# Optimization experiments

Hardware: AMD Instinct MI355X
Metric: run time of the kernel (lower is better)

Reference implementation:

```python
import jax, jax.numpy as jnp
import numpy as np
import math

W = 256      # attention_window
DIL = 1      # attention_dilation
H = 12       # num heads
HD = 64      # head dim
E = 768      # hidden size


def setup_inputs() -> dict:
    key = jax.random.key(0)
    ks = jax.random.split(key, 4)
    B, S = 2, 4096
    s = 0.02
    inp = {"hidden_states": jax.random.normal(ks[0], (B, S, E), jnp.float32)}
    inp["Wq"] = jax.random.normal(ks[1], (E, E), jnp.float32) * s
    inp["Wk"] = jax.random.normal(ks[2], (E, E), jnp.float32) * s
    inp["Wv"] = jax.random.normal(ks[3], (E, E), jnp.float32) * s
    inp["bq"] = jnp.zeros((E,), jnp.float32)
    inp["bk"] = jnp.zeros((E,), jnp.float32)
    inp["bv"] = jnp.zeros((E,), jnp.float32)
    return inp


def _banded_attention(q, k, v):
    # q,k,v: [B,S,H,HD]; banded attention with window W, dilation DIL
    B, S, Hh, D = q.shape
    offsets = (jnp.arange(2 * W + 1) - W) * DIL  # relative key offsets
    pos = jnp.arange(S)

    def score(off):
        idx = pos + off
        valid = (idx >= 0) & (idx < S)          # mask_invalid_locations
        kk = k[:, jnp.clip(idx, 0, S - 1)]      # [B,S,H,HD] shifted keys
        s = jnp.einsum('bshd,bshd->bsh', q, kk)
        return jnp.where(valid[None, :, None], s, -jnp.inf)

    # diagonaled_mm(q, k): [2W+1, B, S, H] -> [B, S, H, 2W+1]
    scores = jax.lax.map(score, offsets)
    probs = jax.nn.softmax(jnp.moveaxis(scores, 0, -1), axis=-1)

    # diagonaled_mm(probs, v, is_t1_diagonaled=True): accumulate over band
    def step(acc, j):
        off = offsets[j]
        idx = pos + off
        valid = (idx >= 0) & (idx < S)
        vv = v[:, jnp.clip(idx, 0, S - 1)]
        p = jnp.where(valid[None, :, None], probs[..., j], 0.0)
        return acc + p[..., None] * vv, None

    out, _ = jax.lax.scan(step, jnp.zeros_like(v), jnp.arange(2 * W + 1))
    return out


def reference(hidden_states, Wq, bq, Wk, bk, Wv, bv):
    B, S, _ = hidden_states.shape
    q = (hidden_states @ Wq.T + bq) / math.sqrt(HD)
    k = hidden_states @ Wk.T + bk
    v = hidden_states @ Wv.T + bv
    q = q.reshape(B, S, H, HD)
    k = k.reshape(B, S, H, HD)
    v = v.reshape(B, S, H, HD)
    out = _banded_attention(q, k, v)  # [B,S,H,HD]
    return out.reshape(B, S, E)
```

## Files before the change

kernel.cpp:

```cpp
#include <hip/hip_runtime.h>

#define S_LEN 4096
#define BATCH 2
#define EMB   768
#define NH    12
#define HDIM  64
#define WIN   256

using f32x4  = __attribute__((ext_vector_type(4))) float;
using bf16x8 = __attribute__((ext_vector_type(8))) short;
using u16x8  = __attribute__((ext_vector_type(8))) unsigned short;

#define AS1 __attribute__((address_space(1)))
#define AS3 __attribute__((address_space(3)))

__device__ __forceinline__ unsigned short f2bf(float x) {
    unsigned int u = __float_as_uint(x);
    return (unsigned short)((u + 0x7fffu + ((u >> 16) & 1u)) >> 16);
}

__global__ void cvt_kernel(const float* __restrict__ in,
                           unsigned short* __restrict__ out, int n8) {
    int i = blockIdx.x * blockDim.x + threadIdx.x;
    if (i >= n8) return;
    const float4* p = reinterpret_cast<const float4*>(in) + (size_t)i * 2;
    float4 a = p[0];
    float4 b = p[1];
    u16x8 o;
    o[0] = f2bf(a.x); o[1] = f2bf(a.y); o[2] = f2bf(a.z); o[3] = f2bf(a.w);
    o[4] = f2bf(b.x); o[5] = f2bf(b.y); o[6] = f2bf(b.z); o[7] = f2bf(b.w);
    reinterpret_cast<u16x8*>(out)[i] = o;
}

__global__ void cvt3_kernel(const float* __restrict__ w0, const float* __restrict__ w1,
                            const float* __restrict__ w2,
                            unsigned short* __restrict__ o0, unsigned short* __restrict__ o1,
                            unsigned short* __restrict__ o2, int n8) {
    int i = blockIdx.x * blockDim.x + threadIdx.x;
    if (i >= n8) return;
    const float* in = (blockIdx.y == 0) ? w0 : (blockIdx.y == 1) ? w1 : w2;
    unsigned short* out = (blockIdx.y == 0) ? o0 : (blockIdx.y == 1) ? o1 : o2;
    const float4* p = reinterpret_cast<const float4*>(in) + (size_t)i * 2;
    float4 a = p[0];
    float4 b = p[1];
    u16x8 o;
    o[0] = f2bf(a.x); o[1] = f2bf(a.y); o[2] = f2bf(a.z); o[3] = f2bf(a.w);
    o[4] = f2bf(b.x); o[5] = f2bf(b.y); o[6] = f2bf(b.z); o[7] = f2bf(b.w);
    reinterpret_cast<u16x8*>(out)[i] = o;
}

#define NKT (EMB / 32)

__global__ __launch_bounds__(256) void qkv_gemm(
    const unsigned short* __restrict__ A,
    const unsigned short* __restrict__ Wq,
    const unsigned short* __restrict__ Wk,
    const unsigned short* __restrict__ Wv,
    const float* __restrict__ bq,
    const float* __restrict__ bk,
    const float* __restrict__ bv,
    unsigned short* __restrict__ qo,
    unsigned short* __restrict__ ko,
    unsigned short* __restrict__ vo)
{
    __shared__ unsigned short As[4][128 * 32];
    __shared__ unsigned short Bs[4][128 * 32];

    const int tid  = threadIdx.x;
    const int lane = tid & 63;
    const int wave = tid >> 6;
    const int mblk = blockIdx.x;
    const int nblk = blockIdx.y;
    const int wsel = nblk / 6;
    const int nloc0 = (nblk % 6) * 128;
    const unsigned short* Wp = (wsel == 0) ? Wq : ((wsel == 1) ? Wk : Wv);
    const int wm = wave >> 1, wn = wave & 1;

    f32x4 acc[4][4];
#pragma unroll
    for (int i = 0; i < 4; ++i)
#pragma unroll
        for (int j = 0; j < 4; ++j)
            acc[i][j] = (f32x4){0.f, 0.f, 0.f, 0.f};

    const int frow = lane & 15;
    const int g    = lane >> 4;

    const char* Abase = (const char*)(A  + (size_t)(mblk * 128) * EMB);
    const char* Bbase = (const char*)(Wp + (size_t)nloc0 * EMB);

    const int srow = tid >> 2;
    const int pb   = tid & 3;
    const int sblk = pb ^ (srow & 3);

#define GLDS(gp, lp) __builtin_amdgcn_global_load_lds((const AS1 unsigned int*)(gp), (AS3 unsigned int*)(lp), 16, 0, 0)
#define STG_A(q, t) do {                                                                                 \
    GLDS(Abase + (size_t)srow * 1536 + (t) * 64 + sblk * 16,        &As[q][srow * 32 + pb * 8]);         \
    GLDS(Abase + (size_t)(64 + srow) * 1536 + (t) * 64 + sblk * 16, &As[q][(64 + srow) * 32 + pb * 8]);  \
} while (0)
#define STG_B(q, t) do {                                                                                 \
    GLDS(Bbase + (size_t)srow * 1536 + (t) * 64 + sblk * 16,        &Bs[q][srow * 32 + pb * 8]);         \
    GLDS(Bbase + (size_t)(64 + srow) * 1536 + (t) * 64 + sblk * 16, &Bs[q][(64 + srow) * 32 + pb * 8]);  \
} while (0)

    auto rdA = [&](int q, int mi) -> bf16x8 {
        int r = wm * 64 + mi * 16 + frow;
        return *reinterpret_cast<const bf16x8*>(&As[q][r * 32 + (g ^ (r & 3)) * 8]);
    };
    auto rdB = [&](int q, int ni) -> bf16x8 {
        int r = wn * 64 + ni * 16 + frow;
        return *reinterpret_cast<const bf16x8*>(&Bs[q][r * 32 + (g ^ (r & 3)) * 8]);
    };

    STG_A(0, 0); STG_B(0, 0);
    STG_A(1, 1); STG_B(1, 1);
    STG_A(2, 2); STG_B(2, 2);
    asm volatile("s_waitcnt vmcnt(8)" ::: "memory");
    asm volatile("s_barrier" ::: "memory");

#define WINDOW(t, DO_STAGE) do {                                                              \
    const int q_ = (t) & 3;                                                                   \
    bf16x8 afr[4], bfr[4];                                                                    \
    _Pragma("unroll") for (int ni = 0; ni < 4; ++ni) bfr[ni] = rdB(q_, ni);                   \
    _Pragma("unroll") for (int mi = 0; mi < 4; ++mi) afr[mi] = rdA(q_, mi);                   \
    if (DO_STAGE) { STG_A(((t) + 3) & 3, (t) + 3); STG_B(((t) + 3) & 3, (t) + 3); }           \
    __builtin_amdgcn_s_setprio(1);                                                            \
    _Pragma("unroll") for (int mi = 0; mi < 4; ++mi)                                          \
        _Pragma("unroll") for (int ni = 0; ni < 4; ++ni)                                      \
            acc[mi][ni] = __builtin_amdgcn_mfma_f32_16x16x32_bf16(afr[mi], bfr[ni], acc[mi][ni], 0, 0, 0); \
    __builtin_amdgcn_s_setprio(0);                                                            \
} while (0)

#pragma unroll 1
    for (int t = 0; t < NKT - 3; ++t) {
        WINDOW(t, true);
        asm volatile("s_waitcnt vmcnt(8)" ::: "memory");
        asm volatile("s_barrier" ::: "memory");
    }
    WINDOW(NKT - 3, false);
    asm volatile("s_waitcnt vmcnt(4)" ::: "memory");
    asm volatile("s_barrier" ::: "memory");
    WINDOW(NKT - 2, false);
    asm volatile("s_waitcnt vmcnt(0)" ::: "memory");
    asm volatile("s_barrier" ::: "memory");
    WINDOW(NKT - 1, false);

    const float* bias = (wsel == 0) ? bq : ((wsel == 1) ? bk : bv);
    const int rowg = g * 4;
#pragma unroll
    for (int mi = 0; mi < 4; ++mi) {
        int mbase = mblk * 128 + wm * 64 + mi * 16 + rowg;
#pragma unroll
        for (int ni = 0; ni < 4; ++ni) {
            int nl = nloc0 + wn * 64 + ni * 16 + frow;
            float bb = bias[nl];
            int h = nl >> 6, hd = nl & 63;
#pragma unroll
            for (int r = 0; r < 4; ++r) {
                int mm = mbase + r;
                int b = mm >> 12, s = mm & 4095;
                float v = acc[mi][ni][r] + bb;
                if (wsel == 0) {
                    v *= 0.125f;
                    qo[((size_t)(b * NH + h) * S_LEN + s) * HDIM + hd] = f2bf(v);
                } else if (wsel == 1) {
                    ko[((size_t)(b * NH + h) * S_LEN + s) * HDIM + hd] = f2bf(v);
                } else {
                    vo[((size_t)(b * NH + h) * HDIM + hd) * S_LEN + s] = f2bf(v);
                }
            }
        }
    }
}

#define QB   128
#define KC   64
#define NCHQ ((QB + 2 * WIN) / KC)

#define STAGE_ATT(buf, ks) do {                                                              \
    const unsigned short* kr_ = kp + (size_t)((ks) + srow) * HDIM + gblk * 8;                \
    __builtin_amdgcn_global_load_lds(                                                        \
        (const AS1 unsigned int*)kr_,                                                        \
        (AS3 unsigned int*)&Ksm[buf][wave * 512], 16, 0, 0);                                 \
    const unsigned short* vr_ = vp + (size_t)srow * S_LEN + (ks) + gblk * 8;                 \
    __builtin_amdgcn_global_load_lds(                                                        \
        (const AS1 unsigned int*)vr_,                                                        \
        (AS3 unsigned int*)&Vsm[buf][wave * 512], 16, 0, 0);                                 \
} while (0)

__global__ __launch_bounds__(512) void banded_attn(
    const unsigned short* __restrict__ qg,
    const unsigned short* __restrict__ kg,
    const unsigned short* __restrict__ vtg,
    float* __restrict__ out)
{
    __shared__ unsigned short Ksm[2][KC * HDIM];
    __shared__ unsigned short Vsm[2][HDIM * KC];
    __shared__ unsigned short Psm[8][16 * KC];

    const int tid  = threadIdx.x;
    const int wave = tid >> 6, lane = tid & 63;
    const int qb = blockIdx.x * QB;
    const int h  = blockIdx.y, b = blockIdx.z;

    const unsigned short* qp = qg  + (size_t)(b * NH + h) * S_LEN * HDIM;
    const unsigned short* kp = kg  + (size_t)(b * NH + h) * S_LEN * HDIM;
    const unsigned short* vp = vtg + (size_t)(b * NH + h) * HDIM * S_LEN;

    const int frow = lane & 15;
    const int g    = lane >> 4;
    const int fcol = g * 8;

    const int srow = tid >> 3;
    const int gblk = (tid & 7) ^ (srow & 7);

    bf16x8 qf[2];
    {
        const unsigned short* qr = qp + (size_t)(qb + wave * 16 + frow) * HDIM;
        qf[0] = *reinterpret_cast<const bf16x8*>(qr + fcol);
        qf[1] = *reinterpret_cast<const bf16x8*>(qr + 32 + fcol);
    }

    float l_part[4];
    f32x4 o_acc[4];
#pragma unroll
    for (int r = 0; r < 4; ++r) l_part[r] = 0.f;
#pragma unroll
    for (int ni = 0; ni < 4; ++ni) o_acc[ni] = (f32x4){0.f, 0.f, 0.f, 0.f};

    const int c_start = (qb < WIN) ? ((WIN - qb) >> 6) : 0;
    const int c_end   = min(NCHQ, (S_LEN + WIN - qb) >> 6);
    const int qrow0 = qb + wave * 16 + g * 4;

    const int w_lo = qb + wave * 16 - WIN;
    const int w_hi = qb + wave * 16 + 15 + WIN;

    STAGE_ATT(0, qb - WIN + c_start * KC);
    asm volatile("s_waitcnt vmcnt(0)" ::: "memory");
    __syncthreads();

    int cur = 0;
    for (int c = c_start; c < c_end; ++c) {
        const int ks = qb - WIN + c * KC;
        if (c + 1 < c_end) STAGE_ATT(cur ^ 1, ks + KC);

        const bool active = (ks + KC - 1 >= w_lo) && (ks <= w_hi);
        if (active) {
            f32x4 sc[4];
#pragma unroll
            for (int ni = 0; ni < 4; ++ni) sc[ni] = (f32x4){0.f, 0.f, 0.f, 0.f};
#pragma unroll
            for (int ni = 0; ni < 4; ++ni) {
                int krow = ni * 16 + frow;
                int sw   = (krow & 7) << 3;
                bf16x8 kf0 = *reinterpret_cast<const bf16x8*>(&Ksm[cur][krow * KC + (fcol ^ sw)]);
                bf16x8 kf1 = *reinterpret_cast<const bf16x8*>(&Ksm[cur][krow * KC + ((32 + fcol) ^ sw)]);
                sc[ni] = __builtin_amdgcn_mfma_f32_16x16x32_bf16(qf[0], kf0, sc[ni], 0, 0, 0);
                sc[ni] = __builtin_amdgcn_mfma_f32_16x16x32_bf16(qf[1], kf1, sc[ni], 0, 0, 0);
            }

            float pm[4][4];
#pragma unroll
            for (int ni = 0; ni < 4; ++ni) {
                int d0 = qrow0 - (ks + ni * 16 + frow);
#pragma unroll
                for (int r = 0; r < 4; ++r) {
                    bool valid = (unsigned)(d0 + r + WIN) <= (unsigned)(2 * WIN);
                    pm[ni][r] = valid ? __expf(sc[ni][r]) : 0.f;
                }
            }
#pragma unroll
            for (int r = 0; r < 4; ++r) {
                l_part[r] += (pm[0][r] + pm[1][r]) + (pm[2][r] + pm[3][r]);
                int prow = g * 4 + r;
#pragma unroll
                for (int ni = 0; ni < 4; ++ni) {
                    int pelem = (ni * 16 + frow) ^ ((prow & 7) << 3);
                    Psm[wave][prow * KC + pelem] = f2bf(pm[ni][r]);
                }
            }

            asm volatile("s_waitcnt lgkmcnt(0)" ::: "memory");
            __builtin_amdgcn_sched_barrier(0);

            bf16x8 pf[2];
#pragma unroll
            for (int kk = 0; kk < 2; ++kk) {
                int sw = (frow & 7) << 3;
                pf[kk] = *reinterpret_cast<const bf16x8*>(&Psm[wave][frow * KC + ((kk * 32 + fcol) ^ sw)]);
            }
#pragma unroll
            for (int ni = 0; ni < 4; ++ni) {
                int vrow = ni * 16 + frow;
                int sw   = (vrow & 7) << 3;
#pragma unroll
                for (int kk = 0; kk < 2; ++kk) {
                    bf16x8 vf = *reinterpret_cast<const bf16x8*>(&Vsm[cur][vrow * KC + ((kk * 32 + fcol) ^ sw)]);
                    o_acc[ni] = __builtin_amdgcn_mfma_f32_16x16x32_bf16(pf[kk], vf, o_acc[ni], 0, 0, 0);
                }
            }
        }

        asm volatile("s_waitcnt vmcnt(0)" ::: "memory");
        __syncthreads();
        cur ^= 1;
    }

#pragma unroll
    for (int d = 1; d < 16; d <<= 1)
#pragma unroll
        for (int r = 0; r < 4; ++r)
            l_part[r] += __shfl_xor(l_part[r], d, 64);

#pragma unroll
    for (int r = 0; r < 4; ++r) {
        float inv = 1.0f / l_part[r];
        int s = qrow0 + r;
        size_t obase = ((size_t)b * S_LEN + s) * EMB + h * HDIM;
#pragma unroll
        for (int ni = 0; ni < 4; ++ni)
            out[obase + ni * 16 + frow] = o_acc[ni][r] * inv;
    }
}

extern "C" void kernel_launch(void* const* d_in, const int* in_sizes, int n_in,
                              void* d_out, int out_size, void* d_ws, size_t ws_size,
                              hipStream_t stream) {
    const float* hs = (const float*)d_in[0];
    const float* Wq = (const float*)d_in[1];
    const float* Wk = (const float*)d_in[2];
    const float* Wv = (const float*)d_in[3];
    const float* bq = (const float*)d_in[4];
    const float* bk = (const float*)d_in[5];
    const float* bv = (const float*)d_in[6];
    float* out = (float*)d_out;

    char* w = (char*)d_ws;
    unsigned short* hs_bf = (unsigned short*)w;
    unsigned short* wq_bf = (unsigned short*)(w + 12582912);
    unsigned short* wk_bf = wq_bf + 589824;
    unsigned short* wv_bf = wk_bf + 589824;
    unsigned short* q_ws  = (unsigned short*)(w + 12582912 + 3 * 1179648);
    unsigned short* k_ws  = q_ws + 6291456;
    unsigned short* v_ws  = k_ws + 6291456;

    cvt_kernel<<<3072, 256, 0, stream>>>(hs, hs_bf, 786432);
    cvt3_kernel<<<dim3(288, 3), 256, 0, stream>>>(Wq, Wk, Wv, wq_bf, wk_bf, wv_bf, 73728);

    qkv_gemm<<<dim3(64, 18), 256, 0, stream>>>(hs_bf, wq_bf, wk_bf, wv_bf,
                                               bq, bk, bv, q_ws, k_ws, v_ws);

    banded_attn<<<dim3(S_LEN / QB, NH, BATCH), 512, 0, stream>>>(q_ws, k_ws, v_ws, out);
}
```

Before: 109.4 us.

## Rework QKV GEMM: swizzled block order, double buffering, vectorized transposed epilogue stores

The QKV projection GEMM remaps workgroup IDs so consecutive blocks share operand tiles in cache. It also changes the LDS swizzle pattern and replaces the 4-deep global_load_lds pipeline with a simpler double buffer that waits on vmcnt(0) each step. For Q and K it swaps the MFMA operand order, and for V it keeps the original order, so each lane holds 4 contiguous output elements. The epilogue can then write packed 4x bf16 stores instead of scalar 16-bit stores. The shallower pipeline and full waits each iteration may expose more load latency, while the halved LDS footprint may allow more resident blocks.

```diff
diff --git a/kernel.cpp b/kernel.cpp
--- a/kernel.cpp
+++ b/kernel.cpp
@@ -9,6 +9,7 @@
 
 using f32x4  = __attribute__((ext_vector_type(4))) float;
 using bf16x8 = __attribute__((ext_vector_type(8))) short;
+using u16x4  = __attribute__((ext_vector_type(4))) unsigned short;
 using u16x8  = __attribute__((ext_vector_type(8))) unsigned short;
 
 #define AS1 __attribute__((address_space(1)))
@@ -63,14 +64,17 @@
     unsigned short* __restrict__ ko,
     unsigned short* __restrict__ vo)
 {
-    __shared__ unsigned short As[4][128 * 32];
-    __shared__ unsigned short Bs[4][128 * 32];
+    __shared__ unsigned short As[2][128 * 32];
+    __shared__ unsigned short Bs[2][128 * 32];
 
     const int tid  = threadIdx.x;
     const int lane = tid & 63;
     const int wave = tid >> 6;
-    const int mblk = blockIdx.x;
-    const int nblk = blockIdx.y;
+
+    const int wg  = blockIdx.y * 64 + blockIdx.x;
+    const int v   = (wg & 7) * 144 + (wg >> 3);
+    const int mblk = v & 63;
+    const int nblk = v >> 6;
     const int wsel = nblk / 6;
     const int nloc0 = (nblk % 6) * 128;
     const unsigned short* Wp = (wsel == 0) ? Wq : ((wsel == 1) ? Wk : Wv);
@@ -91,83 +95,90 @@
 
     const int srow = tid >> 2;
     const int pb   = tid & 3;
-    const int sblk = pb ^ (srow & 3);
+    const int sblk = pb ^ ((srow >> 1) & 3);
 
 #define GLDS(gp, lp) __builtin_amdgcn_global_load_lds((const AS1 unsigned int*)(gp), (AS3 unsigned int*)(lp), 16, 0, 0)
-#define STG_A(q, t) do {                                                                                 \
+#define STG(q, t) do {                                                                                   \
     GLDS(Abase + (size_t)srow * 1536 + (t) * 64 + sblk * 16,        &As[q][srow * 32 + pb * 8]);         \
     GLDS(Abase + (size_t)(64 + srow) * 1536 + (t) * 64 + sblk * 16, &As[q][(64 + srow) * 32 + pb * 8]);  \
-} while (0)
-#define STG_B(q, t) do {                                                                                 \
     GLDS(Bbase + (size_t)srow * 1536 + (t) * 64 + sblk * 16,        &Bs[q][srow * 32 + pb * 8]);         \
     GLDS(Bbase + (size_t)(64 + srow) * 1536 + (t) * 64 + sblk * 16, &Bs[q][(64 + srow) * 32 + pb * 8]);  \
 } while (0)
 
     auto rdA = [&](int q, int mi) -> bf16x8 {
         int r = wm * 64 + mi * 16 + frow;
-        return *reinterpret_cast<const bf16x8*>(&As[q][r * 32 + (g ^ (r & 3)) * 8]);
+        return *reinterpret_cast<const bf16x8*>(&As[q][r * 32 + (g ^ ((r >> 1) & 3)) * 8]);
     };
     auto rdB = [&](int q, int ni) -> bf16x8 {
         int r = wn * 64 + ni * 16 + frow;
-        return *reinterpret_cast<const bf16x8*>(&Bs[q][r * 32 + (g ^ (r & 3)) * 8]);
+        return *reinterpret_cast<const bf16x8*>(&Bs[q][r * 32 + (g ^ ((r >> 1) & 3)) * 8]);
     };
 
-    STG_A(0, 0); STG_B(0, 0);
-    STG_A(1, 1); STG_B(1, 1);
-    STG_A(2, 2); STG_B(2, 2);
-    asm volatile("s_waitcnt vmcnt(8)" ::: "memory");
-    asm volatile("s_barrier" ::: "memory");
-
-#define WINDOW(t, DO_STAGE) do {                                                              \
-    const int q_ = (t) & 3;                                                                   \
-    bf16x8 afr[4], bfr[4];                                                                    \
-    _Pragma("unroll") for (int ni = 0; ni < 4; ++ni) bfr[ni] = rdB(q_, ni);                   \
-    _Pragma("unroll") for (int mi = 0; mi < 4; ++mi) afr[mi] = rdA(q_, mi);                   \
-    if (DO_STAGE) { STG_A(((t) + 3) & 3, (t) + 3); STG_B(((t) + 3) & 3, (t) + 3); }           \
-    __builtin_amdgcn_s_setprio(1);                                                            \
-    _Pragma("unroll") for (int mi = 0; mi < 4; ++mi)                                          \
-        _Pragma("unroll") for (int ni = 0; ni < 4; ++ni)                                      \
-            acc[mi][ni] = __builtin_amdgcn_mfma_f32_16x16x32_bf16(afr[mi], bfr[ni], acc[mi][ni], 0, 0, 0); \
-    __builtin_amdgcn_s_setprio(0);                                                            \
+#define KLOOP(SW) do {                                                                        \
+    STG(0, 0);                                                                                \
+    asm volatile("s_waitcnt vmcnt(0)" ::: "memory");                                          \
+    __syncthreads();                                                                          \
+    int cur = 0;                                                                              \
+    _Pragma("unroll 1")                                                                       \
+    for (int t = 0; t < NKT; ++t) {                                                           \
+        if (t + 1 < NKT) STG(cur ^ 1, t + 1);                                                 \
+        bf16x8 afr[4], bfr[4];                                                                \
+        _Pragma("unroll") for (int ni = 0; ni < 4; ++ni) bfr[ni] = rdB(cur, ni);              \
+        _Pragma("unroll") for (int mi = 0; mi < 4; ++mi) afr[mi] = rdA(cur, mi);              \
+        __builtin_amdgcn_s_setprio(1);                                                        \
+        _Pragma("unroll") for (int mi = 0; mi < 4; ++mi)                                      \
+            _Pragma("unroll") for (int ni = 0; ni < 4; ++ni)                                  \
+                acc[mi][ni] = (SW)                                                            \
+                    ? __builtin_amdgcn_mfma_f32_16x16x32_bf16(bfr[ni], afr[mi], acc[mi][ni], 0, 0, 0)  \
+                    : __builtin_amdgcn_mfma_f32_16x16x32_bf16(afr[mi], bfr[ni], acc[mi][ni], 0, 0, 0); \
+        __builtin_amdgcn_s_setprio(0);                                                        \
+        if (t + 1 < NKT) {                                                                    \
+            asm volatile("s_waitcnt vmcnt(0)" ::: "memory");                                  \
+            __syncthreads();                                                                  \
+            cur ^= 1;                                                                         \
+        }                                                                                     \
+    }                                                                                         \
 } while (0)
 
-#pragma unroll 1
-    for (int t = 0; t < NKT - 3; ++t) {
-        WINDOW(t, true);
-        asm volatile("s_waitcnt vmcnt(8)" ::: "memory");
-        asm volatile("s_barrier" ::: "memory");
-    }
-    WINDOW(NKT - 3, false);
-    asm volatile("s_waitcnt vmcnt(4)" ::: "memory");
-    asm volatile("s_barrier" ::: "memory");
-    WINDOW(NKT - 2, false);
-    asm volatile("s_waitcnt vmcnt(0)" ::: "memory");
-    asm volatile("s_barrier" ::: "memory");
-    WINDOW(NKT - 1, false);
-
-    const float* bias = (wsel == 0) ? bq : ((wsel == 1) ? bk : bv);
-    const int rowg = g * 4;
-#pragma unroll
-    for (int mi = 0; mi < 4; ++mi) {
-        int mbase = mblk * 128 + wm * 64 + mi * 16 + rowg;
-#pragma unroll
-        for (int ni = 0; ni < 4; ++ni) {
-            int nl = nloc0 + wn * 64 + ni * 16 + frow;
-            float bb = bias[nl];
-            int h = nl >> 6, hd = nl & 63;
-#pragma unroll
-            for (int r = 0; r < 4; ++r) {
-                int mm = mbase + r;
-                int b = mm >> 12, s = mm & 4095;
-                float v = acc[mi][ni][r] + bb;
-                if (wsel == 0) {
-                    v *= 0.125f;
-                    qo[((size_t)(b * NH + h) * S_LEN + s) * HDIM + hd] = f2bf(v);
-                } else if (wsel == 1) {
-                    ko[((size_t)(b * NH + h) * S_LEN + s) * HDIM + hd] = f2bf(v);
-                } else {
-                    vo[((size_t)(b * NH + h) * HDIM + hd) * S_LEN + s] = f2bf(v);
-                }
+    if (wsel < 2) {
+        KLOOP(1);
+        const float* bias = (wsel == 0) ? bq : bk;
+        unsigned short* op = (wsel == 0) ? qo : ko;
+        const float qs = (wsel == 0) ? 0.125f : 1.0f;
+#pragma unroll
+        for (int mi = 0; mi < 4; ++mi) {
+            int m = mblk * 128 + wm * 64 + mi * 16 + frow;
+            int b = m >> 12, s = m & 4095;
+#pragma unroll
+            for (int ni = 0; ni < 4; ++ni) {
+                int n0 = nloc0 + wn * 64 + ni * 16 + g * 4;
+                float4 bb = *reinterpret_cast<const float4*>(&bias[n0]);
+                int h = n0 >> 6, hd0 = n0 & 63;
+                u16x4 pk;
+                pk[0] = f2bf((acc[mi][ni][0] + bb.x) * qs);
+                pk[1] = f2bf((acc[mi][ni][1] + bb.y) * qs);
+                pk[2] = f2bf((acc[mi][ni][2] + bb.z) * qs);
+                pk[3] = f2bf((acc[mi][ni][3] + bb.w) * qs);
+                *reinterpret_cast<u16x4*>(&op[((size_t)(b * NH + h) * S_LEN + s) * HDIM + hd0]) = pk;
+            }
+        }
+    } else {
+        KLOOP(0);
+#pragma unroll
+        for (int mi = 0; mi < 4; ++mi) {
+            int m0 = mblk * 128 + wm * 64 + mi * 16 + g * 4;
+            int b = m0 >> 12, s0 = m0 & 4095;
+#pragma unroll
+            for (int ni = 0; ni < 4; ++ni) {
+                int n = nloc0 + wn * 64 + ni * 16 + frow;
+                float bb = bv[n];
+                int h = n >> 6, hd = n & 63;
+                u16x4 pk;
+                pk[0] = f2bf(acc[mi][ni][0] + bb);
+                pk[1] = f2bf(acc[mi][ni][1] + bb);
+                pk[2] = f2bf(acc[mi][ni][2] + bb);
+                pk[3] = f2bf(acc[mi][ni][3] + bb);
+                *reinterpret_cast<u16x4*>(&vo[((size_t)(b * NH + h) * HDIM + hd) * S_LEN + s0]) = pk;
             }
         }
     }
```

Measured after the change: 102.4 us. 1.07x faster.
